# Kernel tuning notes

Hardware: AMD Instinct MI355X
Metric: run time of the kernel (lower is better)

## Reference

```python
import jax, jax.numpy as jnp
import numpy as np

NQ, NK, D = 256, 2048, 128

def setup_inputs() -> dict:
    key = jax.random.key(0)
    ks = jax.random.split(key, 12)
    s = lambda fan_in: 1.0 / np.sqrt(fan_in)
    inp = {
        "x": jax.random.normal(ks[0], (1, D, NQ), jnp.float32),
        "source": jax.random.normal(ks[1], (1, D, NK), jnp.float32),
        "dist": jax.random.normal(ks[2], (1, D, NQ * NK), jnp.float32),
        "mask": jax.random.randint(ks[3], (1, NQ, NK), 0, 2).astype(bool),
        # MLPAttention scoring MLP: Conv1d(384->128,k=1) + ReLU + Conv1d(128->1,k=1)
        "w1": jax.random.uniform(ks[4], (D, 3 * D), jnp.float32, -s(3 * D), s(3 * D)),
        "b1": jax.random.uniform(ks[5], (D,), jnp.float32, -s(3 * D), s(3 * D)),
        "w2": jax.random.uniform(ks[6], (1, D), jnp.float32, -s(D), s(D)),
        "b2": jax.random.uniform(ks[7], (1,), jnp.float32, -s(D), s(D)),
        # AttentionalPropagation MLP: Conv1d(256->256,k=1) + ReLU + Conv1d(256->128,k=1), last bias = 0
        "w3": jax.random.uniform(ks[8], (2 * D, 2 * D), jnp.float32, -s(2 * D), s(2 * D)),
        "b3": jax.random.uniform(ks[9], (2 * D,), jnp.float32, -s(2 * D), s(2 * D)),
        "w4": jax.random.uniform(ks[10], (D, 2 * D), jnp.float32, -s(2 * D), s(2 * D)),
        "b4": jnp.zeros((D,), jnp.float32),
    }
    return inp


def reference(x, source, dist, mask, w1, b1, w2, b2, w3, b3, w4, b4):
    b, d, nq = x.shape
    nk = source.shape[-1]
    # Conv1d(k=1) on concat(q_bcast, k_bcast, dist) == split-weight matmuls (same math, no giant concat)
    wq, wk, wd = w1[:, :d], w1[:, d:2 * d], w1[:, 2 * d:]
    qh = jnp.einsum('oc,bcn->bon', wq, x)                      # [b,d,nq]
    kh = jnp.einsum('oc,bcm->bom', wk, source)                 # [b,d,nk]
    dh = jnp.einsum('oc,bcnm->bonm', wd, dist.reshape(b, d, nq, nk))  # [b,d,nq,nk]
    h = jax.nn.relu(qh[:, :, :, None] + kh[:, :, None, :] + dh + b1[None, :, None, None])
    scores = jnp.einsum('c,bcnm->bnm', w2[0], h) + b2[0]       # [b,nq,nk]
    # boolean mask branch: scores + (min - 20) * (~mask)
    neg = jax.lax.stop_gradient(scores.min()) - 20.0
    scores = scores + neg * (~mask).astype(scores.dtype)
    prob = jax.nn.softmax(scores, axis=-1)
    message = jnp.einsum('bnm,bdm->bdn', prob, source)         # value == source
    # output MLP on concat([x, message], channel dim)
    cat = jnp.concatenate([x, message], axis=1)                # [b,2d,nq]
    hid = jax.nn.relu(jnp.einsum('oc,bcn->bon', w3, cat) + b3[None, :, None])
    out = jnp.einsum('oc,bcn->bon', w4, hid) + b4[None, :, None]
    return out, scores
```

## Files before the change

### kernel.cpp

```cpp
#include <hip/hip_runtime.h>
#include <hip/hip_bf16.h>

#define D_ 128
#define NQ_ 256
#define NK_ 2048
#define P_TOT (NQ_ * NK_)

typedef float f32x4 __attribute__((ext_vector_type(4)));
typedef short bf16x8 __attribute__((ext_vector_type(8)));

__device__ __forceinline__ unsigned short f2bf(float x) {
    union { float f; unsigned u; } v; v.f = x;
    unsigned r = v.u + 0x7FFFu + ((v.u >> 16) & 1u);
    return (unsigned short)(r >> 16);
}

__device__ __forceinline__ void gload16(const float* g, float* l) {
    __builtin_amdgcn_global_load_lds((const __attribute__((address_space(1))) void*)g,
                                     (__attribute__((address_space(3))) void*)l, 16, 0, 0);
}

#define WAITVM_(n) asm volatile("s_waitcnt vmcnt(" #n ")" ::: "memory")
#define WAITVM(n) WAITVM_(n)

__global__ __launch_bounds__(256) void k_prep(
    const float* __restrict__ w1, const float* __restrict__ x,
    const float* __restrict__ b1, const float* __restrict__ src,
    const float* __restrict__ w3, const float* __restrict__ b3,
    float* __restrict__ qb, float* __restrict__ kh, float* __restrict__ p1,
    unsigned* __restrict__ minw) {
    int b = blockIdx.x, t = threadIdx.x;
    if (b == 0 && t == 0) *minw = 0xFFFFFFFFu;
    if (b < 128) {
        int o = b, n = t;
        const float* wr = w1 + o * 384;
        float acc = b1[o];
#pragma unroll 4
        for (int c = 0; c < 128; ++c) acc = fmaf(wr[c], x[c * 256 + n], acc);
        qb[o * 256 + n] = acc;
    } else if (b < 1152) {
        int idx = (b - 128) * 256 + t;
        int o = idx >> 11, m = idx & 2047;
        const float* wr = w1 + o * 384 + 128;
        float acc = 0.f;
#pragma unroll 4
        for (int c = 0; c < 128; ++c) acc = fmaf(wr[c], src[c * 2048 + m], acc);
        kh[o * 2048 + m] = acc;
    } else {
        int o = b - 1152, n = t;
        const float* wr = w3 + o * 256;
        float acc = b3[o];
#pragma unroll 4
        for (int c = 0; c < 128; ++c) acc = fmaf(wr[c], x[c * 256 + n], acc);
        p1[o * 256 + n] = acc;
    }
}

__global__ __launch_bounds__(512, 2) void k_scores(
    const float* __restrict__ dist, const float* __restrict__ w1,
    const float* __restrict__ qb, const float* __restrict__ kh,
    const float* __restrict__ w2, const float* __restrict__ b2,
    float* __restrict__ scores, unsigned* __restrict__ minw) {
    __shared__ __align__(16) float lds[33920];
    float* bufs = lds + 8192;
    float* qbT  = lds + 32768;
    float* w2l  = lds + 33792;

    const int tid = threadIdx.x;
    const int l = tid & 63, wid = tid >> 6;
    const int lg = l >> 4, c16 = l & 15;
    const int mb = blockIdx.x & 7, nb = blockIdx.x >> 3;
    const int m0 = mb * 256, n0 = nb * 8;

    {
        bf16x8* ldsA = (bf16x8*)lds;
#pragma unroll
        for (int i = 0; i < 4; ++i) {
            int s = tid + i * 512;
            int o = s >> 4, oct = s & 15;
            const float* gp = w1 + o * 384 + 256 + oct * 8;
            float4 f0 = *(const float4*)gp;
            float4 f1 = *(const float4*)(gp + 4);
            union { bf16x8 v; unsigned short u[8]; } pk;
            pk.u[0] = f2bf(f0.x); pk.u[1] = f2bf(f0.y); pk.u[2] = f2bf(f0.z); pk.u[3] = f2bf(f0.w);
            pk.u[4] = f2bf(f1.x); pk.u[5] = f2bf(f1.y); pk.u[6] = f2bf(f1.z); pk.u[7] = f2bf(f1.w);
            int mt = o >> 4, kt = oct >> 2;
            int lane2 = ((oct & 3) << 4) | (o & 15);
            ldsA[(mt * 4 + kt) * 64 + lane2] = pk.v;
        }
    }
#pragma unroll
    for (int jj = 0; jj < 2; ++jj) {
        int e = tid + jj * 512;
        int o = e >> 3, nl2 = e & 7;
        qbT[nl2 * 128 + o] = qb[o * 256 + n0 + nl2];
    }
    if (tid < 128) w2l[tid] = w2[tid];

    unsigned khp[2][16];
#pragma unroll
    for (int s = 0; s < 2; ++s) {
        const float* kp = kh + (size_t)(m0 + wid * 32 + s * 16 + c16);
#pragma unroll
        for (int mt = 0; mt < 8; ++mt) {
            float a0 = kp[(size_t)(mt * 16 + lg * 4) * 2048];
            float a1 = kp[(size_t)(mt * 16 + lg * 4 + 1) * 2048];
            float a2 = kp[(size_t)(mt * 16 + lg * 4 + 2) * 2048];
            float a3 = kp[(size_t)(mt * 16 + lg * 4 + 3) * 2048];
            khp[s][mt * 2]     = (unsigned)f2bf(a0) | ((unsigned)f2bf(a1) << 16);
            khp[s][mt * 2 + 1] = (unsigned)f2bf(a2) | ((unsigned)f2bf(a3) << 16);
        }
    }
    __syncthreads();
    WAITVM(0);
    __builtin_amdgcn_sched_barrier(0);

    f32x4 acc[2][8];
#pragma unroll
    for (int s = 0; s < 2; ++s)
#pragma unroll
        for (int mt = 0; mt < 8; ++mt) acc[s][mt] = (f32x4){0.f, 0.f, 0.f, 0.f};

    const float b2v = b2[0];
    float runmin = 1e30f;

    auto issueT = [&](int t, float* buf) {
        int n_l = t >> 2;
        int cq = t & 3;
        const float* basep = dist + (size_t)(n0 + n_l) * 2048 + (size_t)m0;
#pragma unroll
        for (int j = 0; j < 4; ++j) {
            int row = wid * 4 + j;
            int x = ((row >> 3) & 1) << 2;
            gload16(basep + (size_t)(cq * 32 + row) * (size_t)P_TOT + ((l ^ x) << 2),
                    buf + row * 256);
        }
    };

    auto epi = [&](int nl) {
        const float* qr = qbT + nl * 128;
        float sc2[2];
#pragma unroll
        for (int s = 0; s < 2; ++s) {
            float sp = 0.f;
#pragma unroll
            for (int mt = 0; mt < 8; ++mt) {
                unsigned k01 = khp[s][mt * 2];
                unsigned k23 = khp[s][mt * 2 + 1];
                float kh0 = __uint_as_float(k01 << 16);
                float kh1 = __uint_as_float(k01 & 0xffff0000u);
                float kh2 = __uint_as_float(k23 << 16);
                float kh3 = __uint_as_float(k23 & 0xffff0000u);
                int o = mt * 16 + lg * 4;
                float4 qv = *(const float4*)(qr + o);
                float4 wv = *(const float4*)(w2l + o);
                float t0 = fmaxf(acc[s][mt][0] + qv.x + kh0, 0.f);
                float t1 = fmaxf(acc[s][mt][1] + qv.y + kh1, 0.f);
                float t2 = fmaxf(acc[s][mt][2] + qv.z + kh2, 0.f);
                float t3 = fmaxf(acc[s][mt][3] + qv.w + kh3, 0.f);
                sp = fmaf(wv.x, t0, sp); sp = fmaf(wv.y, t1, sp);
                sp = fmaf(wv.z, t2, sp); sp = fmaf(wv.w, t3, sp);
                acc[s][mt] = (f32x4){0.f, 0.f, 0.f, 0.f};
            }
            sp += __shfl_xor(sp, 16);
            sp += __shfl_xor(sp, 32);
            sc2[s] = sp + b2v;
        }
        float wv = (l < 16) ? sc2[0] : sc2[1];
        if (l < 32) scores[(size_t)(n0 + nl) * 2048 + (size_t)(m0 + wid * 32) + l] = wv;
        float mn = fminf(sc2[0], sc2[1]);
        mn = fminf(mn, __shfl_xor(mn, 1));
        mn = fminf(mn, __shfl_xor(mn, 2));
        mn = fminf(mn, __shfl_xor(mn, 4));
        mn = fminf(mn, __shfl_xor(mn, 8));
        runmin = fminf(runmin, mn);
    };

    float* pF = bufs;
    float* pM = bufs + 8192;
    float* pB = bufs + 16384;
    issueT(0, pF); issueT(1, pM); issueT(2, pB);

#define STEP(CQ, NL, DO_ISSUE, VM)                                               \
    {                                                                            \
        WAITVM(VM);                                                              \
        __builtin_amdgcn_sched_barrier(0);                                       \
        __builtin_amdgcn_s_barrier();                                            \
        const bf16x8* ldsAv = (const bf16x8*)lds;                                \
        bf16x8 af[8];                                                            \
        _Pragma("unroll")                                                        \
        for (int mt = 0; mt < 8; ++mt) af[mt] = ldsAv[(mt * 4 + (CQ)) * 64 + l]; \
        _Pragma("unroll")                                                        \
        for (int s = 0; s < 2; ++s) {                                            \
            const int grpx = (wid * 8 + s * 4 + (c16 >> 2)) ^ ((lg & 1) << 2);   \
            const float* rp = pF + lg * 2048 + grpx * 4 + (c16 & 3);             \
            float tv[8];                                                         \
            _Pragma("unroll")                                                    \
            for (int b = 0; b < 8; ++b) tv[b] = rp[b * 256];                     \
            union { unsigned d[4]; bf16x8 v; } bb;                               \
            _Pragma("unroll")                                                    \
            for (int i = 0; i < 4; ++i) {                                        \
                unsigned r0 = __float_as_uint(tv[2 * i])     + 0x8000u;          \
                unsigned r1 = __float_as_uint(tv[2 * i + 1]) + 0x8000u;          \
                bb.d[i] = __builtin_amdgcn_perm(r1, r0, 0x07060302u);            \
            }                                                                    \
            _Pragma("unroll")                                                    \
            for (int mt = 0; mt < 8; ++mt)                                       \
                acc[s][mt] = __builtin_amdgcn_mfma_f32_16x16x32_bf16(            \
                    af[mt], bb.v, acc[s][mt], 0, 0, 0);                          \
        }                                                                        \
        if ((CQ) == 3) epi(NL);                                                  \
        __builtin_amdgcn_s_barrier();                                            \
        if (DO_ISSUE) issueT((NL) * 4 + (CQ) + 3, pF);                           \
        float* t_ = pF; pF = pM; pM = pB; pB = t_;                               \
    }

    for (int nl = 0; nl < 7; ++nl) {
        STEP(0, nl, true, 8)
        STEP(1, nl, true, 8)
        STEP(2, nl, true, 8)
        STEP(3, nl, true, 8)
    }
    STEP(0, 7, true,  8)
    STEP(1, 7, false, 8)
    STEP(2, 7, false, 4)
    STEP(3, 7, false, 0)
#undef STEP

    union { float f; unsigned u; } e; e.f = runmin;
    unsigned key = (e.u & 0x80000000u) ? ~e.u : (e.u | 0x80000000u);
    if (l == 0) atomicMin(minw, key);
}

__global__ __launch_bounds__(256) void k_tail(
    float* __restrict__ scores, const int* __restrict__ mask,
    const float* __restrict__ src, const unsigned* __restrict__ minw,
    const float* __restrict__ w3, const float* __restrict__ w4,
    const float* __restrict__ b4, const float* __restrict__ p1,
    float* __restrict__ out) {
    __shared__ float sc[2][2048];
    __shared__ float red[2][8];
    __shared__ float msgl[2][128];
    __shared__ float hidl[2][256];
    const int t = threadIdx.x, l = t & 63, wv = t >> 6;
    const int n0 = blockIdx.x * 2;

    unsigned key = *minw;
    union { float f; unsigned u; } d;
    d.u = (key & 0x80000000u) ? (key ^ 0x80000000u) : ~key;
    const float neg = d.f - 20.f;

#pragma unroll
    for (int nn = 0; nn < 2; ++nn) {
        int n = n0 + nn;
        float lmax = -1e30f;
#pragma unroll
        for (int i = 0; i < 8; ++i) {
            int m = t + i * 256;
            float v = scores[n * 2048 + m];
            if (!mask[n * 2048 + m]) v += neg;
            scores[n * 2048 + m] = v;
            sc[nn][m] = v;
            lmax = fmaxf(lmax, v);
        }
#pragma unroll
        for (int off = 1; off < 64; off <<= 1) lmax = fmaxf(lmax, __shfl_xor(lmax, off));
        if (l == 0) red[nn][wv] = lmax;
    }
    __syncthreads();
    float smax[2], lsum[2] = {0.f, 0.f};
#pragma unroll
    for (int nn = 0; nn < 2; ++nn)
        smax[nn] = fmaxf(fmaxf(red[nn][0], red[nn][1]), fmaxf(red[nn][2], red[nn][3]));
#pragma unroll
    for (int nn = 0; nn < 2; ++nn) {
#pragma unroll
        for (int i = 0; i < 8; ++i) {
            int m = t + i * 256;
            float e = __expf(sc[nn][m] - smax[nn]);
            sc[nn][m] = e;
            lsum[nn] += e;
        }
#pragma unroll
        for (int off = 1; off < 64; off <<= 1) lsum[nn] += __shfl_xor(lsum[nn], off);
        if (l == 0) red[nn][4 + wv] = lsum[nn];
    }
    __syncthreads();
    const float rinv0 = 1.f / (red[0][4] + red[0][5] + red[0][6] + red[0][7]);
    const float rinv1 = 1.f / (red[1][4] + red[1][5] + red[1][6] + red[1][7]);

    for (int dd = 0; dd < 32; ++dd) {
        int dch = wv * 32 + dd;
        const float* sr = src + dch * 2048;
        float pa = 0.f, pb = 0.f;
#pragma unroll
        for (int j = 0; j < 32; ++j) {
            int mm = l + j * 64;
            float s = sr[mm];
            pa = fmaf(sc[0][mm], s, pa);
            pb = fmaf(sc[1][mm], s, pb);
        }
#pragma unroll
        for (int off = 1; off < 64; off <<= 1) {
            pa += __shfl_xor(pa, off);
            pb += __shfl_xor(pb, off);
        }
        if (l == 0) { msgl[0][dch] = pa * rinv0; msgl[1][dch] = pb * rinv1; }
    }
    __syncthreads();

    {
        int o = t;
        const float* wr = w3 + o * 256 + 128;
        float a0 = p1[o * 256 + n0];
        float a1 = p1[o * 256 + n0 + 1];
#pragma unroll
        for (int c = 0; c < 128; c += 4) {
            float4 w4v = *(const float4*)(wr + c);
            a0 = fmaf(w4v.x, msgl[0][c], a0);     a1 = fmaf(w4v.x, msgl[1][c], a1);
            a0 = fmaf(w4v.y, msgl[0][c + 1], a0); a1 = fmaf(w4v.y, msgl[1][c + 1], a1);
            a0 = fmaf(w4v.z, msgl[0][c + 2], a0); a1 = fmaf(w4v.z, msgl[1][c + 2], a1);
            a0 = fmaf(w4v.w, msgl[0][c + 3], a0); a1 = fmaf(w4v.w, msgl[1][c + 3], a1);
        }
        hidl[0][o] = fmaxf(a0, 0.f);
        hidl[1][o] = fmaxf(a1, 0.f);
    }
    __syncthreads();

    {
        int o = t & 127, nn = t >> 7;
        const float* wr = w4 + o * 256;
        const float* hr = hidl[nn];
        float acc = b4[o];
#pragma unroll
        for (int c = 0; c < 256; c += 4) {
            float4 w4v = *(const float4*)(wr + c);
            acc = fmaf(w4v.x, hr[c], acc);
            acc = fmaf(w4v.y, hr[c + 1], acc);
            acc = fmaf(w4v.z, hr[c + 2], acc);
            acc = fmaf(w4v.w, hr[c + 3], acc);
        }
        out[o * 256 + n0 + nn] = acc;
    }
}

extern "C" void kernel_launch(void* const* d_in, const int* in_sizes, int n_in,
                              void* d_out, int out_size, void* d_ws, size_t ws_size,
                              hipStream_t stream) {
    const float* x      = (const float*)d_in[0];
    const float* source = (const float*)d_in[1];
    const float* dist   = (const float*)d_in[2];
    const int*   mask   = (const int*)d_in[3];
    const float* w1     = (const float*)d_in[4];
    const float* b1     = (const float*)d_in[5];
    const float* w2     = (const float*)d_in[6];
    const float* b2     = (const float*)d_in[7];
    const float* w3     = (const float*)d_in[8];
    const float* b3     = (const float*)d_in[9];
    const float* w4     = (const float*)d_in[10];
    const float* b4     = (const float*)d_in[11];

    float* outp    = (float*)d_out;
    float* scoresp = outp + 32768;

    float* ws   = (float*)d_ws;
    float* qb   = ws;
    float* kh   = ws + 32768;
    float* p1   = ws + 294912;
    unsigned* minw = (unsigned*)(ws + 360448);

    k_prep<<<1408, 256, 0, stream>>>(w1, x, b1, source, w3, b3, qb, kh, p1, minw);
    k_scores<<<256, 512, 0, stream>>>(dist, w1, qb, kh, w2, b2, scoresp, minw);
    k_tail<<<128, 256, 0, stream>>>(scoresp, mask, source, minw, w3, w4, b4, p1, outp);
}
```

Before: 119.8 us.

## Deepen dist prefetch pipeline to seven half-tile LDS slots

Replaces the three-buffer full-tile prefetch of dist chunks with a seven-slot ring of half-tiles (16 channels each), so more global loads stay in flight ahead of the MFMA consumer. The waitcnt thresholds are retuned so each step waits only for its own two half-slots. The goal is to hide more HBM latency on the bandwidth-bound dist stream. In exchange LDS use grows, which may limit occupancy at two blocks per CU, and the vmcnt bookkeeping is fragile.

```diff
diff --git a/kernel.cpp b/kernel.cpp
--- a/kernel.cpp
+++ b/kernel.cpp
@@ -61,10 +61,9 @@
     const float* __restrict__ qb, const float* __restrict__ kh,
     const float* __restrict__ w2, const float* __restrict__ b2,
     float* __restrict__ scores, unsigned* __restrict__ minw) {
-    __shared__ __align__(16) float lds[33920];
-    float* bufs = lds + 8192;
-    float* qbT  = lds + 32768;
-    float* w2l  = lds + 33792;
+    __shared__ __align__(16) float lds[38016];
+    float* qbT = lds + 36864;
+    float* w2l = lds + 37888;
 
     const int tid = threadIdx.x;
     const int l = tid & 63, wid = tid >> 6;
@@ -124,16 +123,15 @@
     const float b2v = b2[0];
     float runmin = 1e30f;
 
-    auto issueT = [&](int t, float* buf) {
-        int n_l = t >> 2;
-        int cq = t & 3;
+    auto issueH = [&](int h, float* buf) {
+        int n_l = h >> 3, kq = (h >> 1) & 3, hf = h & 1;
         const float* basep = dist + (size_t)(n0 + n_l) * 2048 + (size_t)m0;
 #pragma unroll
-        for (int j = 0; j < 4; ++j) {
-            int row = wid * 4 + j;
-            int x = ((row >> 3) & 1) << 2;
-            gload16(basep + (size_t)(cq * 32 + row) * (size_t)P_TOT + ((l ^ x) << 2),
-                    buf + row * 256);
+        for (int j = 0; j < 2; ++j) {
+            int r16 = wid * 2 + j;
+            int ch = kq * 32 + hf * 16 + r16;
+            int x = ((r16 >> 3) & 1) << 2;
+            gload16(basep + (size_t)ch * P_TOT + ((l ^ x) << 2), buf + r16 * 256);
         }
     };
 
@@ -176,12 +174,17 @@
         runmin = fminf(runmin, mn);
     };
 
-    float* pF = bufs;
-    float* pM = bufs + 8192;
-    float* pB = bufs + 16384;
-    issueT(0, pF); issueT(1, pM); issueT(2, pB);
-
-#define STEP(CQ, NL, DO_ISSUE, VM)                                               \
+    float* p0 = lds + 8192;
+    float* p1 = p0 + 4096;
+    float* p2 = p0 + 8192;
+    float* p3 = p0 + 12288;
+    float* p4 = p0 + 16384;
+    float* p5 = p0 + 20480;
+    float* p6 = p0 + 24576;
+    issueH(0, p0); issueH(1, p1); issueH(2, p2); issueH(3, p3);
+    issueH(4, p4); issueH(5, p5); issueH(6, p6);
+
+#define STEP(CQ, NL, NISS, VM)                                                   \
     {                                                                            \
         WAITVM(VM);                                                              \
         __builtin_amdgcn_sched_barrier(0);                                       \
@@ -190,10 +193,11 @@
         bf16x8 af[8];                                                            \
         _Pragma("unroll")                                                        \
         for (int mt = 0; mt < 8; ++mt) af[mt] = ldsAv[(mt * 4 + (CQ)) * 64 + l]; \
+        const float* slotp = (lg < 2) ? p0 : p1;                                 \
         _Pragma("unroll")                                                        \
         for (int s = 0; s < 2; ++s) {                                            \
             const int grpx = (wid * 8 + s * 4 + (c16 >> 2)) ^ ((lg & 1) << 2);   \
-            const float* rp = pF + lg * 2048 + grpx * 4 + (c16 & 3);             \
+            const float* rp = slotp + (lg & 1) * 2048 + grpx * 4 + (c16 & 3);    \
             float tv[8];                                                         \
             _Pragma("unroll")                                                    \
             for (int b = 0; b < 8; ++b) tv[b] = rp[b * 256];                     \
@@ -211,20 +215,26 @@
         }                                                                        \
         if ((CQ) == 3) epi(NL);                                                  \
         __builtin_amdgcn_s_barrier();                                            \
-        if (DO_ISSUE) issueT((NL) * 4 + (CQ) + 3, pF);                           \
-        float* t_ = pF; pF = pM; pM = pB; pB = t_;                               \
-    }
-
-    for (int nl = 0; nl < 7; ++nl) {
-        STEP(0, nl, true, 8)
-        STEP(1, nl, true, 8)
-        STEP(2, nl, true, 8)
-        STEP(3, nl, true, 8)
-    }
-    STEP(0, 7, true,  8)
-    STEP(1, 7, false, 8)
-    STEP(2, 7, false, 4)
-    STEP(3, 7, false, 0)
+        if ((NISS) >= 1) issueH(((NL) * 4 + (CQ)) * 2 + 7, p0);                  \
+        if ((NISS) >= 2) issueH(((NL) * 4 + (CQ)) * 2 + 8, p1);                  \
+        { float* t0_ = p0; float* t1_ = p1;                                      \
+          p0 = p2; p1 = p3; p2 = p4; p3 = p5; p4 = p6; p5 = t0_; p6 = t1_; }     \
+    }
+
+    STEP(0, 0, 2, 10)
+    STEP(1, 0, 2, 10)
+    STEP(2, 0, 2, 10)
+    STEP(3, 0, 2, 10)
+    for (int nl = 1; nl < 7; ++nl) {
+        STEP(0, nl, 2, 11)
+        STEP(1, nl, 2, 11)
+        STEP(2, nl, 2, 10)
+        STEP(3, nl, 2, 10)
+    }
+    STEP(0, 7, 1, 11)
+    STEP(1, 7, 0, 9)
+    STEP(2, 7, 0, 4)
+    STEP(3, 7, 0, 0)
 #undef STEP
 
     union { float f; unsigned u; } e; e.f = runmin;
```

Result: no change. 121.5 us (+1.4%).

## Retile score kernel to 1024-thread blocks with 16-channel pipelined stages

Applied to the files above, without the earlier changes.

The score kernel moves from 512-thread blocks covering 8 queries by 256 keys to 1024-thread blocks covering 4 queries by 512 keys. The channel dimension is now streamed in 16-channel slices through a three-slot LDS ring over 32 stages, using the 16x16x16 bf16 MFMA instead of 16x16x32. The aim is more waves per block and finer-grained overlap of dist loads with compute. In exchange there are twice as many barriers and MFMA issues per unit of data, only one block fits per CU, and each wave has fewer loads in flight.

```diff
diff --git a/kernel.cpp b/kernel.cpp
--- a/kernel.cpp
+++ b/kernel.cpp
@@ -7,7 +7,13 @@
 #define P_TOT (NQ_ * NK_)
 
 typedef float f32x4 __attribute__((ext_vector_type(4)));
-typedef short bf16x8 __attribute__((ext_vector_type(8)));
+typedef short bf16x4 __attribute__((ext_vector_type(4)));
+
+#if __has_builtin(__builtin_amdgcn_mfma_f32_16x16x16_bf16)
+#define MFMA16(a, b, c) __builtin_amdgcn_mfma_f32_16x16x16_bf16((a), (b), (c), 0, 0, 0)
+#else
+#define MFMA16(a, b, c) __builtin_amdgcn_mfma_f32_16x16x16bf16_1k((a), (b), (c), 0, 0, 0)
+#endif
 
 __device__ __forceinline__ unsigned short f2bf(float x) {
     union { float f; unsigned u; } v; v.f = x;
@@ -56,43 +62,39 @@
     }
 }
 
-__global__ __launch_bounds__(512, 2) void k_scores(
+__global__ __launch_bounds__(1024) void k_scores(
     const float* __restrict__ dist, const float* __restrict__ w1,
     const float* __restrict__ qb, const float* __restrict__ kh,
     const float* __restrict__ w2, const float* __restrict__ b2,
     float* __restrict__ scores, unsigned* __restrict__ minw) {
-    __shared__ __align__(16) float lds[33920];
-    float* bufs = lds + 8192;
+    __shared__ __align__(16) float lds[33408];
+    float* ring = lds + 8192;
     float* qbT  = lds + 32768;
-    float* w2l  = lds + 33792;
+    float* w2l  = lds + 33280;
 
     const int tid = threadIdx.x;
-    const int l = tid & 63, wid = tid >> 6;
+    const int l = tid & 63, w = tid >> 6;
     const int lg = l >> 4, c16 = l & 15;
-    const int mb = blockIdx.x & 7, nb = blockIdx.x >> 3;
-    const int m0 = mb * 256, n0 = nb * 8;
+    const int mb = blockIdx.x & 3, nb = blockIdx.x >> 2;
+    const int m0 = mb * 512, n0 = nb * 4;
 
     {
-        bf16x8* ldsA = (bf16x8*)lds;
+        bf16x4* A4 = (bf16x4*)lds;
 #pragma unroll
         for (int i = 0; i < 4; ++i) {
-            int s = tid + i * 512;
-            int o = s >> 4, oct = s & 15;
-            const float* gp = w1 + o * 384 + 256 + oct * 8;
-            float4 f0 = *(const float4*)gp;
-            float4 f1 = *(const float4*)(gp + 4);
-            union { bf16x8 v; unsigned short u[8]; } pk;
-            pk.u[0] = f2bf(f0.x); pk.u[1] = f2bf(f0.y); pk.u[2] = f2bf(f0.z); pk.u[3] = f2bf(f0.w);
-            pk.u[4] = f2bf(f1.x); pk.u[5] = f2bf(f1.y); pk.u[6] = f2bf(f1.z); pk.u[7] = f2bf(f1.w);
-            int mt = o >> 4, kt = oct >> 2;
-            int lane2 = ((oct & 3) << 4) | (o & 15);
-            ldsA[(mt * 4 + kt) * 64 + lane2] = pk.v;
-        }
-    }
-#pragma unroll
-    for (int jj = 0; jj < 2; ++jj) {
-        int e = tid + jj * 512;
-        int o = e >> 3, nl2 = e & 7;
+            int e = tid + i * 1024;
+            int le = e & 63, kt = (e >> 6) & 7, mt = e >> 9;
+            int o = mt * 16 + (le & 15);
+            int ch = kt * 16 + (le >> 4) * 4;
+            float4 f = *(const float4*)(w1 + o * 384 + 256 + ch);
+            union { unsigned d[2]; bf16x4 v; } pk;
+            pk.d[0] = (unsigned)f2bf(f.x) | ((unsigned)f2bf(f.y) << 16);
+            pk.d[1] = (unsigned)f2bf(f.z) | ((unsigned)f2bf(f.w) << 16);
+            A4[e] = pk.v;
+        }
+    }
+    if (tid < 512) {
+        int o = tid >> 2, nl2 = tid & 3;
         qbT[nl2 * 128 + o] = qb[o * 256 + n0 + nl2];
     }
     if (tid < 128) w2l[tid] = w2[tid];
@@ -100,7 +102,7 @@
     unsigned khp[2][16];
 #pragma unroll
     for (int s = 0; s < 2; ++s) {
-        const float* kp = kh + (size_t)(m0 + wid * 32 + s * 16 + c16);
+        const float* kp = kh + (size_t)(m0 + w * 32 + s * 16 + c16);
 #pragma unroll
         for (int mt = 0; mt < 8; ++mt) {
             float a0 = kp[(size_t)(mt * 16 + lg * 4) * 2048];
@@ -124,17 +126,21 @@
     const float b2v = b2[0];
     float runmin = 1e30f;
 
-    auto issueT = [&](int t, float* buf) {
-        int n_l = t >> 2;
-        int cq = t & 3;
-        const float* basep = dist + (size_t)(n0 + n_l) * 2048 + (size_t)m0;
-#pragma unroll
-        for (int j = 0; j < 4; ++j) {
-            int row = wid * 4 + j;
-            int x = ((row >> 3) & 1) << 2;
-            gload16(basep + (size_t)(cq * 32 + row) * (size_t)P_TOT + ((l ^ x) << 2),
-                    buf + row * 256);
-        }
+    const int keyw = ((w >> 2) & 1) << 2;
+    const int key2 = (lg & 1) << 2;
+    const int hmo = (w >> 3) * 256 + (c16 & 3);
+    const int q0 = (w & 7) * 8 + (c16 >> 2);
+    const int off0 = hmo + ((q0 ^ key2) << 2);
+    const int off1 = hmo + (((q0 + 4) ^ key2) << 2);
+
+    auto issueS = [&](int T, float* buf) {
+        int nl = T >> 3, kt = T & 7;
+        const float* g = dist + (size_t)(kt * 16 + w) * P_TOT
+                              + (size_t)(n0 + nl) * 2048 + (size_t)m0
+                              + (size_t)((l ^ keyw) << 2);
+        float* d = buf + w * 512;
+        gload16(g, d);
+        gload16(g + 256, d + 256);
     };
 
     auto epi = [&](int nl) {
@@ -167,7 +173,7 @@
             sc2[s] = sp + b2v;
         }
         float wv = (l < 16) ? sc2[0] : sc2[1];
-        if (l < 32) scores[(size_t)(n0 + nl) * 2048 + (size_t)(m0 + wid * 32) + l] = wv;
+        if (l < 32) scores[(size_t)(n0 + nl) * 2048 + (size_t)(m0 + w * 32) + l] = wv;
         float mn = fminf(sc2[0], sc2[1]);
         mn = fminf(mn, __shfl_xor(mn, 1));
         mn = fminf(mn, __shfl_xor(mn, 2));
@@ -176,55 +182,48 @@
         runmin = fminf(runmin, mn);
     };
 
-    float* pF = bufs;
-    float* pM = bufs + 8192;
-    float* pB = bufs + 16384;
-    issueT(0, pF); issueT(1, pM); issueT(2, pB);
-
-#define STEP(CQ, NL, DO_ISSUE, VM)                                               \
+    issueS(0, ring); issueS(1, ring + 8192); issueS(2, ring + 16384);
+
+#define STEP(T, POS, NISS, VM)                                                   \
     {                                                                            \
         WAITVM(VM);                                                              \
         __builtin_amdgcn_sched_barrier(0);                                       \
         __builtin_amdgcn_s_barrier();                                            \
-        const bf16x8* ldsAv = (const bf16x8*)lds;                                \
-        bf16x8 af[8];                                                            \
+        const bf16x4* A4 = (const bf16x4*)lds;                                   \
+        bf16x4 af[8];                                                            \
         _Pragma("unroll")                                                        \
-        for (int mt = 0; mt < 8; ++mt) af[mt] = ldsAv[(mt * 4 + (CQ)) * 64 + l]; \
+        for (int mt = 0; mt < 8; ++mt) af[mt] = A4[(mt * 8 + ((T) & 7)) * 64 + l]; \
+        const float* sp_ = ring + (POS) * 8192;                                  \
         _Pragma("unroll")                                                        \
         for (int s = 0; s < 2; ++s) {                                            \
-            const int grpx = (wid * 8 + s * 4 + (c16 >> 2)) ^ ((lg & 1) << 2);   \
-            const float* rp = pF + lg * 2048 + grpx * 4 + (c16 & 3);             \
-            float tv[8];                                                         \
+            const int offs = s ? off1 : off0;                                    \
+            float tv[4];                                                         \
             _Pragma("unroll")                                                    \
-            for (int b = 0; b < 8; ++b) tv[b] = rp[b * 256];                     \
-            union { unsigned d[4]; bf16x8 v; } bb;                               \
-            _Pragma("unroll")                                                    \
-            for (int i = 0; i < 4; ++i) {                                        \
-                unsigned r0 = __float_as_uint(tv[2 * i])     + 0x8000u;          \
-                unsigned r1 = __float_as_uint(tv[2 * i + 1]) + 0x8000u;          \
-                bb.d[i] = __builtin_amdgcn_perm(r1, r0, 0x07060302u);            \
-            }                                                                    \
+            for (int b = 0; b < 4; ++b) tv[b] = sp_[((lg * 4 + b) << 9) + offs]; \
+            union { unsigned d[2]; bf16x4 v; } bb;                               \
+            bb.d[0] = __builtin_amdgcn_perm(__float_as_uint(tv[1]) + 0x8000u,    \
+                                            __float_as_uint(tv[0]) + 0x8000u,    \
+                                            0x07060302u);                        \
+            bb.d[1] = __builtin_amdgcn_perm(__float_as_uint(tv[3]) + 0x8000u,    \
+                                            __float_as_uint(tv[2]) + 0x8000u,    \
+                                            0x07060302u);                        \
             _Pragma("unroll")                                                    \
             for (int mt = 0; mt < 8; ++mt)                                       \
-                acc[s][mt] = __builtin_amdgcn_mfma_f32_16x16x32_bf16(            \
-                    af[mt], bb.v, acc[s][mt], 0, 0, 0);                          \
+                acc[s][mt] = MFMA16(af[mt], bb.v, acc[s][mt]);                   \
         }                                                                        \
-        if ((CQ) == 3) epi(NL);                                                  \
+        if (((T) & 7) == 7) epi((T) >> 3);                                       \
         __builtin_amdgcn_s_barrier();                                            \
-        if (DO_ISSUE) issueT((NL) * 4 + (CQ) + 3, pF);                           \
-        float* t_ = pF; pF = pM; pM = pB; pB = t_;                               \
-    }
-
-    for (int nl = 0; nl < 7; ++nl) {
-        STEP(0, nl, true, 8)
-        STEP(1, nl, true, 8)
-        STEP(2, nl, true, 8)
-        STEP(3, nl, true, 8)
-    }
-    STEP(0, 7, true,  8)
-    STEP(1, 7, false, 8)
-    STEP(2, 7, false, 4)
-    STEP(3, 7, false, 0)
+        if (NISS) issueS((T) + 3, ring + ((T) % 3) * 8192);                      \
+    }
+
+    STEP(0, 0, 1, 4)  STEP(1, 1, 1, 4)  STEP(2, 2, 1, 4)  STEP(3, 0, 1, 4)
+    STEP(4, 1, 1, 4)  STEP(5, 2, 1, 4)  STEP(6, 0, 1, 4)  STEP(7, 1, 1, 4)
+    STEP(8, 2, 1, 4)  STEP(9, 0, 1, 4)  STEP(10, 1, 1, 4) STEP(11, 2, 1, 4)
+    STEP(12, 0, 1, 4) STEP(13, 1, 1, 4) STEP(14, 2, 1, 4) STEP(15, 0, 1, 4)
+    STEP(16, 1, 1, 4) STEP(17, 2, 1, 4) STEP(18, 0, 1, 4) STEP(19, 1, 1, 4)
+    STEP(20, 2, 1, 4) STEP(21, 0, 1, 4) STEP(22, 1, 1, 4) STEP(23, 2, 1, 4)
+    STEP(24, 0, 1, 4) STEP(25, 1, 1, 4) STEP(26, 2, 1, 4) STEP(27, 0, 1, 4)
+    STEP(28, 1, 1, 4) STEP(29, 2, 0, 4) STEP(30, 0, 0, 2) STEP(31, 1, 0, 0)
 #undef STEP
 
     union { float f; unsigned u; } e; e.f = runmin;
@@ -370,6 +369,6 @@
     unsigned* minw = (unsigned*)(ws + 360448);
 
     k_prep<<<1408, 256, 0, stream>>>(w1, x, b1, source, w3, b3, qb, kh, p1, minw);
-    k_scores<<<256, 512, 0, stream>>>(dist, w1, qb, kh, w2, b2, scoresp, minw);
+    k_scores<<<256, 1024, 0, stream>>>(dist, w1, qb, kh, w2, b2, scoresp, minw);
     k_tail<<<128, 256, 0, stream>>>(scoresp, mask, source, minw, w3, w4, b4, p1, outp);
 }
```

Result: slower. 252.6 us (+110.8%).

## Stage dist tiles through registers instead of direct global-to-LDS loads

Applied to the files above, without the earlier changes.

Replaces the async global_load_lds prefetch of dist tiles with register-staged loads: each tile is loaded into f32x4 registers three steps ahead, then written to a rotating LDS ring before the barrier. One of the two barriers per step is dropped because the ring is three slots deep. This costs extra VGPRs (48 floats of staging) and adds LDS write traffic, and the compiler's vmcnt waits now happen implicitly at the LDS store. It may reduce occupancy under the 512x2 launch bound.

```diff
diff --git a/kernel.cpp b/kernel.cpp
--- a/kernel.cpp
+++ b/kernel.cpp
@@ -14,14 +14,6 @@
     unsigned r = v.u + 0x7FFFu + ((v.u >> 16) & 1u);
     return (unsigned short)(r >> 16);
 }
-
-__device__ __forceinline__ void gload16(const float* g, float* l) {
-    __builtin_amdgcn_global_load_lds((const __attribute__((address_space(1))) void*)g,
-                                     (__attribute__((address_space(3))) void*)l, 16, 0, 0);
-}
-
-#define WAITVM_(n) asm volatile("s_waitcnt vmcnt(" #n ")" ::: "memory")
-#define WAITVM(n) WAITVM_(n)
 
 __global__ __launch_bounds__(256) void k_prep(
     const float* __restrict__ w1, const float* __restrict__ x,
@@ -62,7 +54,7 @@
     const float* __restrict__ w2, const float* __restrict__ b2,
     float* __restrict__ scores, unsigned* __restrict__ minw) {
     __shared__ __align__(16) float lds[33920];
-    float* bufs = lds + 8192;
+    float* ring = lds + 8192;
     float* qbT  = lds + 32768;
     float* w2l  = lds + 33792;
 
@@ -112,8 +104,6 @@
         }
     }
     __syncthreads();
-    WAITVM(0);
-    __builtin_amdgcn_sched_barrier(0);
 
     f32x4 acc[2][8];
 #pragma unroll
@@ -124,18 +114,17 @@
     const float b2v = b2[0];
     float runmin = 1e30f;
 
-    auto issueT = [&](int t, float* buf) {
-        int n_l = t >> 2;
-        int cq = t & 3;
-        const float* basep = dist + (size_t)(n0 + n_l) * 2048 + (size_t)m0;
-#pragma unroll
-        for (int j = 0; j < 4; ++j) {
-            int row = wid * 4 + j;
-            int x = ((row >> 3) & 1) << 2;
-            gload16(basep + (size_t)(cq * 32 + row) * (size_t)P_TOT + ((l ^ x) << 2),
-                    buf + row * 256);
-        }
-    };
+    f32x4 ldA[4], ldB[4], ldC[4];
+
+#define LOADT(T, LDV)                                                            \
+    {                                                                            \
+        const float* basep_ = dist + (size_t)(n0 + ((T) >> 2)) * 2048            \
+                                   + (size_t)m0 + (size_t)(l << 2);              \
+        _Pragma("unroll")                                                        \
+        for (int j = 0; j < 4; ++j)                                              \
+            LDV[j] = *(const f32x4*)(basep_ +                                    \
+                     (size_t)(((T) & 3) * 32 + wid * 4 + j) * (size_t)P_TOT);    \
+    }
 
     auto epi = [&](int nl) {
         const float* qr = qbT + nl * 128;
@@ -176,24 +165,29 @@
         runmin = fminf(runmin, mn);
     };
 
-    float* pF = bufs;
-    float* pM = bufs + 8192;
-    float* pB = bufs + 16384;
-    issueT(0, pF); issueT(1, pM); issueT(2, pB);
-
-#define STEP(CQ, NL, DO_ISSUE, VM)                                               \
+    LOADT(0, ldA) LOADT(1, ldB) LOADT(2, ldC)
+
+#define STEP(CQ, NL, P, LDV, DO_ISSUE)                                           \
     {                                                                            \
-        WAITVM(VM);                                                              \
+        float* bufw = ring + (P) * 8192;                                         \
+        _Pragma("unroll")                                                        \
+        for (int j = 0; j < 4; ++j) {                                            \
+            int row_ = wid * 4 + j;                                              \
+            int x_ = ((row_ >> 3) & 1) << 2;                                     \
+            *(f32x4*)(bufw + row_ * 256 + ((l ^ x_) << 2)) = LDV[j];             \
+        }                                                                        \
+        asm volatile("s_waitcnt lgkmcnt(0)" ::: "memory");                       \
         __builtin_amdgcn_sched_barrier(0);                                       \
         __builtin_amdgcn_s_barrier();                                            \
         const bf16x8* ldsAv = (const bf16x8*)lds;                                \
         bf16x8 af[8];                                                            \
         _Pragma("unroll")                                                        \
         for (int mt = 0; mt < 8; ++mt) af[mt] = ldsAv[(mt * 4 + (CQ)) * 64 + l]; \
+        const float* cur = ring + (P) * 8192;                                    \
         _Pragma("unroll")                                                        \
         for (int s = 0; s < 2; ++s) {                                            \
             const int grpx = (wid * 8 + s * 4 + (c16 >> 2)) ^ ((lg & 1) << 2);   \
-            const float* rp = pF + lg * 2048 + grpx * 4 + (c16 & 3);             \
+            const float* rp = cur + lg * 2048 + grpx * 4 + (c16 & 3);            \
             float tv[8];                                                         \
             _Pragma("unroll")                                                    \
             for (int b = 0; b < 8; ++b) tv[b] = rp[b * 256];                     \
@@ -210,22 +204,19 @@
                     af[mt], bb.v, acc[s][mt], 0, 0, 0);                          \
         }                                                                        \
         if ((CQ) == 3) epi(NL);                                                  \
-        __builtin_amdgcn_s_barrier();                                            \
-        if (DO_ISSUE) issueT((NL) * 4 + (CQ) + 3, pF);                           \
-        float* t_ = pF; pF = pM; pM = pB; pB = t_;                               \
-    }
-
-    for (int nl = 0; nl < 7; ++nl) {
-        STEP(0, nl, true, 8)
-        STEP(1, nl, true, 8)
-        STEP(2, nl, true, 8)
-        STEP(3, nl, true, 8)
-    }
-    STEP(0, 7, true,  8)
-    STEP(1, 7, false, 8)
-    STEP(2, 7, false, 4)
-    STEP(3, 7, false, 0)
+        if (DO_ISSUE) LOADT((NL) * 4 + (CQ) + 3, LDV)                            \
+    }
+
+    STEP(0, 0, 0, ldA, 1) STEP(1, 0, 1, ldB, 1) STEP(2, 0, 2, ldC, 1) STEP(3, 0, 0, ldA, 1)
+    STEP(0, 1, 1, ldB, 1) STEP(1, 1, 2, ldC, 1) STEP(2, 1, 0, ldA, 1) STEP(3, 1, 1, ldB, 1)
+    STEP(0, 2, 2, ldC, 1) STEP(1, 2, 0, ldA, 1) STEP(2, 2, 1, ldB, 1) STEP(3, 2, 2, ldC, 1)
+    STEP(0, 3, 0, ldA, 1) STEP(1, 3, 1, ldB, 1) STEP(2, 3, 2, ldC, 1) STEP(3, 3, 0, ldA, 1)
+    STEP(0, 4, 1, ldB, 1) STEP(1, 4, 2, ldC, 1) STEP(2, 4, 0, ldA, 1) STEP(3, 4, 1, ldB, 1)
+    STEP(0, 5, 2, ldC, 1) STEP(1, 5, 0, ldA, 1) STEP(2, 5, 1, ldB, 1) STEP(3, 5, 2, ldC, 1)
+    STEP(0, 6, 0, ldA, 1) STEP(1, 6, 1, ldB, 1) STEP(2, 6, 2, ldC, 1) STEP(3, 6, 0, ldA, 1)
+    STEP(0, 7, 1, ldB, 1) STEP(1, 7, 2, ldC, 0) STEP(2, 7, 0, ldA, 0) STEP(3, 7, 1, ldB, 0)
 #undef STEP
+#undef LOADT
 
     union { float f; unsigned u; } e; e.f = runmin;
     unsigned key = (e.u & 0x80000000u) ? ~e.u : (e.u | 0x80000000u);
```

Result: slower. 147.9 us (+23.4%).
